# Kernel tuning notes

Measured on AMD Instinct MI355X. Metric: run time of the kernel, lower is better.

## Reference

```python
import jax, jax.numpy as jnp
import numpy as np

NDIM = 3
RADIUS = 0.14
MAX_GRID_DIM = 96
MAX_COLLISIONS = 128
B, N, M, C = 4, 4096, 4096, 16


def setup_inputs() -> dict:
    key = jax.random.key(0)
    k1, k2, k3 = jax.random.split(key, 3)
    locs = jax.random.uniform(k1, (B, N, NDIM), dtype=jnp.float32)
    data = jax.random.normal(k2, (B, N, C), dtype=jnp.float32)
    qlocs = jax.random.uniform(k3, (B, M, NDIM), dtype=jnp.float32)
    return {"locs": locs, "data": data, "qlocs": qlocs}


def _hashgrid_idxs(locs, radius, max_grid_dim):
    """Replicates hashgrid_order: assign each particle a flat grid-cell ID and
    return the permutation (new -> old index) that sorts particles by cell."""
    lower = locs.min(axis=1)                                   # [B,D]
    upper = locs.max(axis=1)                                   # [B,D]
    grid_dims = jnp.ceil(jnp.clip((upper - lower) / radius, 0.0, max_grid_dim))
    center = (lower + upper) * 0.5
    lower = center - grid_dims * radius * 0.5                  # grid lower corner
    cell = jnp.floor((locs - lower[:, None, :]) / radius)
    cell = jnp.clip(cell, 0.0, grid_dims[:, None, :] - 1.0).astype(jnp.int32)
    gd = jnp.maximum(grid_dims.astype(jnp.int32), 1)           # [B,D]
    # row-major strides per batch: stride[d] = prod(gd[d+1:])
    rev = jnp.cumprod(gd[:, ::-1], axis=1)[:, ::-1]            # [B,D]
    strides = jnp.concatenate(
        [rev[:, 1:], jnp.ones((gd.shape[0], 1), jnp.int32)], axis=1)
    cell_ids = (cell * strides[:, None, :]).sum(-1)            # [B,N]
    # stable sort by cell id -> idxs[b, i] = original index of particle now at i
    idxs = jnp.argsort(cell_ids, axis=1)
    return idxs


def reference(locs, data, qlocs):
    idxs = _hashgrid_idxs(locs, RADIUS, MAX_GRID_DIM)
    locs_r = jnp.take_along_axis(locs, idxs[..., None], axis=1)   # [B,N,D]
    data_r = jnp.take_along_axis(data, idxs[..., None], axis=1)   # [B,N,C]

    # Radius search of qlocs against the cell-sorted particles. Neighbor indices
    # are w.r.t. the reordered locs, listed in ascending reordered-index order
    # (cell order), capped at MAX_COLLISIONS, padded with -1.
    qn = (qlocs * qlocs).sum(-1)                                  # [B,M]
    pn = (locs_r * locs_r).sum(-1)                                # [B,N]
    cross = jnp.einsum('bmd,bnd->bmn', qlocs, locs_r)             # [B,M,N]
    dist2 = qn[:, :, None] + pn[:, None, :] - 2.0 * cross         # [B,M,N]
    mask = dist2 <= RADIUS * RADIUS
    # stable argsort of ~mask puts in-radius particles first, in index order
    order = jnp.argsort(~mask, axis=-1)
    neighbors = order[..., :MAX_COLLISIONS].astype(jnp.int32)     # [B,M,K]
    count = mask.sum(-1)                                          # [B,M]
    valid = jnp.arange(MAX_COLLISIONS) < count[..., None]
    neighbors = jnp.where(valid, neighbors, jnp.int32(-1))
    return locs_r, data_r, idxs.astype(jnp.int32), neighbors
```

## Files before the change

### kernel.cpp

```cpp
#include <hip/hip_runtime.h>
#include <stdint.h>

#define BB 4
#define NN 4096
#define MM 4096
#define CC 16
#define KMAX 128

static constexpr int LOCSR_OFF = 0;
static constexpr int DATAR_OFF = BB * NN * 3;
static constexpr int IDXS_OFF  = DATAR_OFF + BB * NN * CC;
static constexpr int NB_OFF    = IDXS_OFF + BB * NN;

static constexpr float RAD_F = 0.14f;
static constexpr float R2F   = (float)(0.14 * 0.14);

static constexpr int MAXC    = 96 * 96 * 96;
static constexpr int CSTRIDE = MAXC + 8;

__global__ void __launch_bounds__(1024) k_bbox(const float* __restrict__ locs,
                                               float* __restrict__ gp) {
    int b = blockIdx.x;
    __shared__ float smn[3][1024], smx[3][1024];
    int t = threadIdx.x;
    float mn[3] = {1e30f, 1e30f, 1e30f}, mx[3] = {-1e30f, -1e30f, -1e30f};
    const float* base = locs + b * NN * 3;
    for (int i = t; i < NN; i += 1024) {
        for (int d = 0; d < 3; ++d) {
            float v = base[i * 3 + d];
            mn[d] = fminf(mn[d], v);
            mx[d] = fmaxf(mx[d], v);
        }
    }
    for (int d = 0; d < 3; ++d) { smn[d][t] = mn[d]; smx[d][t] = mx[d]; }
    __syncthreads();
    for (int s = 512; s > 0; s >>= 1) {
        if (t < s) {
            for (int d = 0; d < 3; ++d) {
                smn[d][t] = fminf(smn[d][t], smn[d][t + s]);
                smx[d][t] = fmaxf(smx[d][t], smx[d][t + s]);
            }
        }
        __syncthreads();
    }
    if (t == 0) {
        float low2[3], gdf[3];
        int gdi[3];
        for (int d = 0; d < 3; ++d) {
            float lo = smn[d][0], up = smx[d][0];
            float u = __fdiv_rn(__fsub_rn(up, lo), RAD_F);
            u = fminf(fmaxf(u, 0.0f), 96.0f);
            float g = ceilf(u);
            float center = __fmul_rn(__fadd_rn(lo, up), 0.5f);
            low2[d] = __fsub_rn(center, __fmul_rn(__fmul_rn(g, RAD_F), 0.5f));
            gdf[d] = g;
            gdi[d] = max((int)g, 1);
        }
        float* o = gp + b * 12;
        o[0] = low2[0]; o[1] = low2[1]; o[2] = low2[2];
        o[3] = gdf[0];  o[4] = gdf[1];  o[5] = gdf[2];
        ((int*)o)[6]  = gdi[1] * gdi[2];
        ((int*)o)[7]  = gdi[2];
        ((int*)o)[8]  = gdi[0] * gdi[1] * gdi[2];
        ((int*)o)[9]  = gdi[0];
        ((int*)o)[10] = gdi[1];
        ((int*)o)[11] = gdi[2];
    }
}

__global__ void k_cellid(const float* __restrict__ locs, const float* __restrict__ gp,
                         int* __restrict__ cid) {
    int idx = blockIdx.x * 256 + threadIdx.x;
    int b = idx >> 12;
    int i = idx & (NN - 1);
    const float* o = gp + b * 12;
    int s0 = ((const int*)o)[6], s1 = ((const int*)o)[7];
    int cc[3];
    for (int d = 0; d < 3; ++d) {
        float x = locs[(b * NN + i) * 3 + d];
        float c = floorf(__fdiv_rn(__fsub_rn(x, o[d]), RAD_F));
        c = fminf(fmaxf(c, 0.0f), __fsub_rn(o[3 + d], 1.0f));
        cc[d] = (int)c;
    }
    cid[b * NN + i] = cc[0] * s0 + cc[1] * s1 + cc[2];
}

__global__ void __launch_bounds__(1024) k_rank(const float* __restrict__ locs,
                                               const float* __restrict__ data,
                                               const int* __restrict__ cid,
                                               float* __restrict__ out,
                                               float4* __restrict__ sp4,
                                               int* __restrict__ cs_sorted) {
    __shared__ int4 keys4[NN / 4];
    __shared__ int partial[16][64];
    __shared__ int s_dst[64];
    int blk = blockIdx.x;
    int b = blk >> 6;
    int t = threadIdx.x;
    int wave = t >> 6, lane = t & 63;
    const int4* kg = (const int4*)(cid + b * NN);
    keys4[t] = kg[t];
    __syncthreads();
    int i = (blk & 63) * 64 + lane;
    int key = ((const int*)keys4)[i];
    int rank = 0;
    int j0 = wave * 64;
#pragma unroll 4
    for (int j4 = j0; j4 < j0 + 64; ++j4) {
        int4 kv = keys4[j4];
        int jb = j4 * 4;
        rank += (kv.x < key) || (kv.x == key && (jb    ) < i);
        rank += (kv.y < key) || (kv.y == key && (jb + 1) < i);
        rank += (kv.z < key) || (kv.z == key && (jb + 2) < i);
        rank += (kv.w < key) || (kv.w == key && (jb + 3) < i);
    }
    partial[wave][lane] = rank;
    __syncthreads();
    if (wave == 0) {
        int r = 0;
#pragma unroll
        for (int w = 0; w < 16; ++w) r += partial[w][lane];
        s_dst[lane] = r;
    }
    __syncthreads();
    if (wave == 0) {
        int src = b * NN + i;
        int dst = b * NN + s_dst[lane];
        float x = locs[src * 3 + 0], y = locs[src * 3 + 1], z = locs[src * 3 + 2];
        out[IDXS_OFF + dst] = (float)i;
        out[LOCSR_OFF + dst * 3 + 0] = x;
        out[LOCSR_OFF + dst * 3 + 1] = y;
        out[LOCSR_OFF + dst * 3 + 2] = z;
        cs_sorted[dst] = key;
        float pn = __fadd_rn(__fadd_rn(__fmul_rn(x, x), __fmul_rn(y, y)), __fmul_rn(z, z));
        sp4[dst] = make_float4(x, y, z, pn);
    } else if (wave <= 4) {
        int p = lane;
        int ii = (blk & 63) * 64 + p;
        int dst = b * NN + s_dst[p];
        int c = wave - 1;
        const float4* dsrc = (const float4*)(data + (b * NN + ii) * 16);
        float4* ddst = (float4*)(out + DATAR_OFF + dst * 16);
        ddst[c] = dsrc[c];
    }
}

__global__ void __launch_bounds__(256) k_cellstart(const int* __restrict__ cs_sorted,
                                                   const float* __restrict__ gp,
                                                   int* __restrict__ cell_start) {
    int b = blockIdx.y;
    int nc = ((const int*)(gp + b * 12))[8];
    const int* cs = cs_sorted + b * NN;
    int* cst = cell_start + b * CSTRIDE;
    for (int c = blockIdx.x * 256 + threadIdx.x; c <= nc; c += gridDim.x * 256) {
        int lo = 0, hi = NN;
        while (lo < hi) {
            int mid = (lo + hi) >> 1;
            if (cs[mid] < c) lo = mid + 1; else hi = mid;
        }
        cst[c] = lo;
    }
}

__device__ inline void axis_range(float qd, float lo, int gd, int* c0, int* c1) {
    const float DL = RAD_F + 1e-4f;
    float vlo = (qd - DL - lo) / RAD_F;
    float vhi = (qd + DL - lo) / RAD_F;
    int a = (int)floorf(vlo), b = (int)floorf(vhi);
    *c0 = min(max(a, 0), gd - 1);
    *c1 = min(max(b, 0), gd - 1);
}

__global__ void __launch_bounds__(256, 8) k_neighbors(const float* __restrict__ qlocs,
                                                      const float4* __restrict__ sp4,
                                                      const int* __restrict__ cell_start,
                                                      const float* __restrict__ gp,
                                                      float* __restrict__ out) {
    int blk = blockIdx.x;
    int b = blk >> 10;
    int wave = threadIdx.x >> 6, lane = threadIdx.x & 63;
    int m = (blk & 1023) * 4 + wave;
    const float* o = gp + b * 12;
    const int* oi = (const int*)o;
    int s0 = oi[6], s1 = oi[7];
    int gd0 = oi[9], gd1 = oi[10], gd2 = oi[11];
    const float* q = qlocs + (b * MM + m) * 3;
    float q0 = q[0], q1 = q[1], q2 = q[2];
    float qn = __fadd_rn(__fadd_rn(__fmul_rn(q0, q0), __fmul_rn(q1, q1)), __fmul_rn(q2, q2));
    int cx0, cx1, cy0, cy1, cz0, cz1;
    axis_range(q0, o[0], gd0, &cx0, &cx1);
    axis_range(q1, o[1], gd1, &cy0, &cy1);
    axis_range(q2, o[2], gd2, &cz0, &cz1);
    const float4* sp = sp4 + b * NN;
    const int* cst = cell_start + b * CSTRIDE;
    float* nb = out + NB_OFF + (b * MM + m) * KMAX;
    int count = 0;
    for (int cx = cx0; cx <= cx1; ++cx) {
        for (int cy = cy0; cy <= cy1; ++cy) {
            int base = cx * s0 + cy * s1;
            int ps = cst[base + cz0];
            int pe = cst[base + cz1 + 1];
            for (int p0 = ps; p0 < pe; p0 += 64) {
                int p = p0 + lane;
                float4 P = sp[p];
                float cross = fmaf(q2, P.z, fmaf(q1, P.y, __fmul_rn(q0, P.x)));
                float dist2 = __fsub_rn(__fadd_rn(qn, P.w), __fmul_rn(2.0f, cross));
                bool hit = (p < pe) && (dist2 <= R2F);
                unsigned long long bal = __ballot(hit);
                if (hit) {
                    int pos = count + __popcll(bal & ((1ull << lane) - 1ull));
                    if (pos < KMAX) nb[pos] = (float)p;
                }
                count += __popcll(bal);
                if (count >= KMAX) goto done;
            }
        }
    }
done:
    for (int j = count + lane; j < KMAX; j += 64) nb[j] = -1.0f;
}

extern "C" void kernel_launch(void* const* d_in, const int* in_sizes, int n_in,
                              void* d_out, int out_size, void* d_ws, size_t ws_size,
                              hipStream_t stream) {
    const float* locs  = (const float*)d_in[0];
    const float* data  = (const float*)d_in[1];
    const float* qlocs = (const float*)d_in[2];
    float* out = (float*)d_out;
    char* ws = (char*)d_ws;
    float* gp        = (float*)ws;
    int*   cid       = (int*)(ws + 512);
    int*   cs_sorted = (int*)(ws + 512 + 65536);
    float4* sp4      = (float4*)(ws + 512 + 2 * 65536);
    int*   cell_start = (int*)(ws + 512 + 2 * 65536 + BB * NN * sizeof(float4));

    k_bbox<<<BB, 1024, 0, stream>>>(locs, gp);
    k_cellid<<<(BB * NN) / 256, 256, 0, stream>>>(locs, gp, cid);
    k_rank<<<BB * 64, 1024, 0, stream>>>(locs, data, cid, out, sp4, cs_sorted);
    k_cellstart<<<dim3(32, BB), 256, 0, stream>>>(cs_sorted, gp, cell_start);
    k_neighbors<<<BB * 1024, 256, 0, stream>>>(qlocs, sp4, cell_start, gp, out);
}
```

Baseline: 100.1 us.

## Fuse cell-id computation into bbox kernel and pack index into sort key

The separate cell-id kernel is merged into the bounding-box kernel, so each batch computes its grid parameters and then writes cell ids from the same block, removing one launch. Each key now packs the cell id shifted left by 12 with the particle index. This makes every key unique, so the rank count becomes a plain less-than compare with no stable tie-break. The rank loop unroll goes from 4 to 8, and cell_start decodes the cell from the key by shifting. In exchange, the cell-id pass now runs on only 4 blocks, and cell ids must fit in 20 bits, which holds for a 96^3 grid.

Result: faster. 93.88 us (-6.2%).

```diff
diff --git a/kernel.cpp b/kernel.cpp
--- a/kernel.cpp
+++ b/kernel.cpp
@@ -18,10 +18,13 @@
 static constexpr int MAXC    = 96 * 96 * 96;
 static constexpr int CSTRIDE = MAXC + 8;
 
-__global__ void __launch_bounds__(1024) k_bbox(const float* __restrict__ locs,
-                                               float* __restrict__ gp) {
+__global__ void __launch_bounds__(1024) k_grid(const float* __restrict__ locs,
+                                               float* __restrict__ gp,
+                                               unsigned* __restrict__ cid) {
     int b = blockIdx.x;
     __shared__ float smn[3][1024], smx[3][1024];
+    __shared__ float sp_low[3], sp_gdf[3];
+    __shared__ int sp_s0, sp_s1;
     int t = threadIdx.x;
     float mn[3] = {1e30f, 1e30f, 1e30f}, mx[3] = {-1e30f, -1e30f, -1e30f};
     const float* base = locs + b * NN * 3;
@@ -65,54 +68,48 @@
         ((int*)o)[9]  = gdi[0];
         ((int*)o)[10] = gdi[1];
         ((int*)o)[11] = gdi[2];
-    }
-}
-
-__global__ void k_cellid(const float* __restrict__ locs, const float* __restrict__ gp,
-                         int* __restrict__ cid) {
-    int idx = blockIdx.x * 256 + threadIdx.x;
-    int b = idx >> 12;
-    int i = idx & (NN - 1);
-    const float* o = gp + b * 12;
-    int s0 = ((const int*)o)[6], s1 = ((const int*)o)[7];
-    int cc[3];
-    for (int d = 0; d < 3; ++d) {
-        float x = locs[(b * NN + i) * 3 + d];
-        float c = floorf(__fdiv_rn(__fsub_rn(x, o[d]), RAD_F));
-        c = fminf(fmaxf(c, 0.0f), __fsub_rn(o[3 + d], 1.0f));
-        cc[d] = (int)c;
-    }
-    cid[b * NN + i] = cc[0] * s0 + cc[1] * s1 + cc[2];
+        for (int d = 0; d < 3; ++d) { sp_low[d] = low2[d]; sp_gdf[d] = gdf[d]; }
+        sp_s0 = gdi[1] * gdi[2];
+        sp_s1 = gdi[2];
+    }
+    __syncthreads();
+    float l0 = sp_low[0], l1 = sp_low[1], l2 = sp_low[2];
+    float g0 = sp_gdf[0], g1 = sp_gdf[1], g2 = sp_gdf[2];
+    int s0 = sp_s0, s1 = sp_s1;
+    for (int i = t; i < NN; i += 1024) {
+        float x0 = base[i * 3 + 0], x1 = base[i * 3 + 1], x2 = base[i * 3 + 2];
+        float c0 = fminf(fmaxf(floorf(__fdiv_rn(__fsub_rn(x0, l0), RAD_F)), 0.0f), __fsub_rn(g0, 1.0f));
+        float c1 = fminf(fmaxf(floorf(__fdiv_rn(__fsub_rn(x1, l1), RAD_F)), 0.0f), __fsub_rn(g1, 1.0f));
+        float c2 = fminf(fmaxf(floorf(__fdiv_rn(__fsub_rn(x2, l2), RAD_F)), 0.0f), __fsub_rn(g2, 1.0f));
+        unsigned cell = (unsigned)((int)c0 * s0 + (int)c1 * s1 + (int)c2);
+        cid[b * NN + i] = cell * 4096u + (unsigned)i;
+    }
 }
 
 __global__ void __launch_bounds__(1024) k_rank(const float* __restrict__ locs,
                                                const float* __restrict__ data,
-                                               const int* __restrict__ cid,
+                                               const unsigned* __restrict__ cid,
                                                float* __restrict__ out,
                                                float4* __restrict__ sp4,
-                                               int* __restrict__ cs_sorted) {
-    __shared__ int4 keys4[NN / 4];
+                                               unsigned* __restrict__ cs_sorted) {
+    __shared__ uint4 keys4[NN / 4];
     __shared__ int partial[16][64];
     __shared__ int s_dst[64];
     int blk = blockIdx.x;
     int b = blk >> 6;
     int t = threadIdx.x;
     int wave = t >> 6, lane = t & 63;
-    const int4* kg = (const int4*)(cid + b * NN);
+    const uint4* kg = (const uint4*)(cid + b * NN);
     keys4[t] = kg[t];
     __syncthreads();
     int i = (blk & 63) * 64 + lane;
-    int key = ((const int*)keys4)[i];
+    unsigned key = ((const unsigned*)keys4)[i];
     int rank = 0;
     int j0 = wave * 64;
-#pragma unroll 4
+#pragma unroll 8
     for (int j4 = j0; j4 < j0 + 64; ++j4) {
-        int4 kv = keys4[j4];
-        int jb = j4 * 4;
-        rank += (kv.x < key) || (kv.x == key && (jb    ) < i);
-        rank += (kv.y < key) || (kv.y == key && (jb + 1) < i);
-        rank += (kv.z < key) || (kv.z == key && (jb + 2) < i);
-        rank += (kv.w < key) || (kv.w == key && (jb + 3) < i);
+        uint4 kv = keys4[j4];
+        rank += (kv.x < key) + (kv.y < key) + (kv.z < key) + (kv.w < key);
     }
     partial[wave][lane] = rank;
     __syncthreads();
@@ -145,18 +142,18 @@
     }
 }
 
-__global__ void __launch_bounds__(256) k_cellstart(const int* __restrict__ cs_sorted,
+__global__ void __launch_bounds__(256) k_cellstart(const unsigned* __restrict__ cs_sorted,
                                                    const float* __restrict__ gp,
                                                    int* __restrict__ cell_start) {
     int b = blockIdx.y;
     int nc = ((const int*)(gp + b * 12))[8];
-    const int* cs = cs_sorted + b * NN;
+    const unsigned* cs = cs_sorted + b * NN;
     int* cst = cell_start + b * CSTRIDE;
     for (int c = blockIdx.x * 256 + threadIdx.x; c <= nc; c += gridDim.x * 256) {
         int lo = 0, hi = NN;
         while (lo < hi) {
             int mid = (lo + hi) >> 1;
-            if (cs[mid] < c) lo = mid + 1; else hi = mid;
+            if ((int)(cs[mid] >> 12) < c) lo = mid + 1; else hi = mid;
         }
         cst[c] = lo;
     }
@@ -228,14 +225,13 @@
     const float* qlocs = (const float*)d_in[2];
     float* out = (float*)d_out;
     char* ws = (char*)d_ws;
-    float* gp        = (float*)ws;
-    int*   cid       = (int*)(ws + 512);
-    int*   cs_sorted = (int*)(ws + 512 + 65536);
-    float4* sp4      = (float4*)(ws + 512 + 2 * 65536);
-    int*   cell_start = (int*)(ws + 512 + 2 * 65536 + BB * NN * sizeof(float4));
-
-    k_bbox<<<BB, 1024, 0, stream>>>(locs, gp);
-    k_cellid<<<(BB * NN) / 256, 256, 0, stream>>>(locs, gp, cid);
+    float*    gp        = (float*)ws;
+    unsigned* cid       = (unsigned*)(ws + 512);
+    unsigned* cs_sorted = (unsigned*)(ws + 512 + 65536);
+    float4*   sp4       = (float4*)(ws + 512 + 2 * 65536);
+    int* cell_start = (int*)(ws + 512 + 2 * 65536 + BB * NN * sizeof(float4));
+
+    k_grid<<<BB, 1024, 0, stream>>>(locs, gp, cid);
     k_rank<<<BB * 64, 1024, 0, stream>>>(locs, data, cid, out, sp4, cs_sorted);
     k_cellstart<<<dim3(32, BB), 256, 0, stream>>>(cs_sorted, gp, cell_start);
     k_neighbors<<<BB * 1024, 256, 0, stream>>>(qlocs, sp4, cell_start, gp, out);
```
